# Kernel optimization log

Hardware: AMD Instinct MI355X
Metric: run time of the kernel (lower is better)

## Reference

```python
import jax, jax.numpy as jnp
import numpy as np

N = 131072        # total packed tokens
D = 256           # input_dim
E = 512           # embed_dim
B = 16            # number of batches (len(cu_seqlens)-1)
NLAYERS = 64      # max distinct layer ids per batch


def setup_inputs() -> dict:
    key = jax.random.key(0)
    ks = jax.random.split(key, 8)
    feats = jax.random.normal(ks[0], (N, D), dtype=jnp.float32)
    cu_seqlens = jnp.arange(0, N + 1, N // B, dtype=jnp.int32)  # [B+1]
    layer_ids = jax.random.randint(ks[1], (N,), 0, NLAYERS, dtype=jnp.int32)
    # Linear params stored as [in, out] (y = x @ W + b), matching torch Linear math.
    Wa = jax.random.normal(ks[2], (D, 1), jnp.float32) * 0.05
    ba = jnp.zeros((1,), jnp.float32)
    W1 = jax.random.normal(ks[3], (3 * D, E), jnp.float32) * 0.02
    b1 = jnp.zeros((E,), jnp.float32)
    W2 = jax.random.normal(ks[4], (E, D), jnp.float32) * 0.02
    b2 = jnp.zeros((D,), jnp.float32)
    Wc = jax.random.normal(ks[5], (2 * D, D), jnp.float32) * 0.02
    bc = jnp.zeros((D,), jnp.float32)
    return dict(feats=feats, cu_seqlens=cu_seqlens, layer_ids=layer_ids,
                Wa=Wa, ba=ba, W1=W1, b1=b1, W2=W2, b2=b2, Wc=Wc, bc=bc)


def _forward(feats, cu_seqlens, layer_ids, Wa, ba, W1, b1, W2, b2, Wc, bc):
    n = feats.shape[0]
    nseg = B * NLAYERS
    # batch id of each token from the cumulative sequence lengths
    batch_ids = jnp.searchsorted(cu_seqlens, jnp.arange(n, dtype=jnp.int32), side='right') - 1
    # global (batch, layer) segment id -> vectorizes the per-batch scatter loop
    seg = batch_ids * NLAYERS + layer_ids

    counts = jax.ops.segment_sum(jnp.ones((n,), feats.dtype), seg, num_segments=nseg)  # [nseg]
    sums = jax.ops.segment_sum(feats, seg, num_segments=nseg)                           # [nseg, D]
    avg_pool = sums / jnp.maximum(counts, 1.0)[:, None]
    max_pool = jax.ops.segment_max(feats, seg, num_segments=nseg)
    max_pool = jnp.where(counts[:, None] > 0, max_pool, 0.0)  # empty segments -> 0 (never gathered)

    # attention softmax over all tokens of each batch (dim=0 within the batch slice)
    logits = (feats @ Wa + ba)[:, 0]                                    # [n]
    m = jax.ops.segment_max(logits, batch_ids, num_segments=B)          # [B]
    e = jnp.exp(logits - m[batch_ids])
    z = jax.ops.segment_sum(e, batch_ids, num_segments=B)               # [B]
    w = e / z[batch_ids]                                                # [n]
    attention_pool = jax.ops.segment_sum(feats * w[:, None], seg, num_segments=nseg)

    pooled = jnp.concatenate([avg_pool, max_pool, attention_pool], axis=1)  # [nseg, 3D]
    h = jax.nn.gelu(pooled @ W1 + b1, approximate=False)
    layer_feats = h @ W2 + b2                                               # [nseg, D]

    gathered = layer_feats[seg]                                             # [n, D]
    out = jnp.concatenate([gathered, feats], axis=1) @ Wc + bc              # [n, D]
    return out


def reference(feats, cu_seqlens, layer_ids, Wa, ba, W1, b1, W2, b2, Wc, bc):
    return _forward(feats, cu_seqlens, layer_ids, Wa, ba, W1, b1, W2, b2, Wc, bc)
```

## Files before the change

### kernel.cpp

```cpp
#include <hip/hip_runtime.h>
#include <hip/hip_bf16.h>
#include <math.h>

#define NTOK 131072
#define DIM  256
#define EDIM 512
#define NB   16
#define NL   64
#define NSEG (NB*NL)
#define K3D  768
#define K2D  512
#define HB   64
#define K4CH 256

typedef __attribute__((ext_vector_type(8))) short short8;
typedef __attribute__((ext_vector_type(4))) float f32x4;

static __device__ __forceinline__ unsigned fcode(float x){
  unsigned b = __float_as_uint(x);
  return (b & 0x80000000u) ? ~b : (b | 0x80000000u);
}
static __device__ __forceinline__ float fdecode(unsigned c){
  unsigned b = (c & 0x80000000u) ? (c ^ 0x80000000u) : ~c;
  return __uint_as_float(b);
}
#define NEG_INF_CODE 0x007FFFFFu

static __device__ __forceinline__ short f2bf(float x){
  union { __hip_bfloat16 h; short s; } u; u.h = __float2bfloat16(x); return u.s;
}
static __device__ __forceinline__ float bf2f(short s){
  union { float f; unsigned u; } u; u.u = ((unsigned)(unsigned short)s) << 16; return u.f;
}

__global__ __launch_bounds__(256) void k0_transpose(const float* __restrict__ W1, const float* __restrict__ W2,
                                                    const float* __restrict__ Wc,
                                                    short* __restrict__ W1t, short* __restrict__ W2t,
                                                    short* __restrict__ Wct, unsigned* __restrict__ bmax,
                                                    int* __restrict__ segcnt){
  if (blockIdx.x == 0){
    if (threadIdx.x < NB) bmax[threadIdx.x] = NEG_INF_CODE;
    for (int i = threadIdx.x; i < NSEG; i += 256) segcnt[i] = 0;
  }
  __shared__ short tile[64][65];
  int b = blockIdx.x;
  const float* src; short* dst; int K, N, kt, nt;
  if (b < 96){ src=W1; dst=W1t; K=768; N=512; kt=b/8;  nt=b%8;  }
  else if (b < 128){ int c=b-96;  src=W2; dst=W2t; K=512; N=256; kt=c/4; nt=c%4; }
  else             { int c=b-128; src=Wc; dst=Wct; K=512; N=256; kt=c/4; nt=c%4; }
  int k0 = kt*64, n0 = nt*64;
  for (int e = threadIdx.x; e < 4096; e += 256){
    int r = e >> 6, c = e & 63;
    tile[c][r] = f2bf(src[(size_t)(k0+r)*N + n0 + c]);
  }
  __syncthreads();
  for (int e = threadIdx.x; e < 4096; e += 256){
    int r = e >> 6, c = e & 63;
    dst[(size_t)(n0+r)*K + k0 + c] = tile[r][c];
  }
}

template<int WRITEB>
__global__ __launch_bounds__(256) void k1_logits(const float* __restrict__ feats, const int* __restrict__ cu,
    const int* __restrict__ layer_ids, const float* __restrict__ Wa, const float* __restrict__ ba,
    float* __restrict__ logits, int* __restrict__ seg, unsigned* __restrict__ bmax,
    short* __restrict__ featsb){
  __shared__ int      lcu[NB];
  __shared__ unsigned lbm[NB];
  int tid = threadIdx.x;
  if (tid < NB){ lcu[tid] = cu[tid+1]; lbm[tid] = NEG_INF_CODE; }
  int s = tid & 15;
  int rowoff = tid >> 4;
  float4 w0 = *(const float4*)(Wa + s*4);
  float4 w1 = *(const float4*)(Wa + 64 + s*4);
  float4 w2 = *(const float4*)(Wa + 128 + s*4);
  float4 w3 = *(const float4*)(Wa + 192 + s*4);
  float bav = ba[0];
  __syncthreads();
#pragma unroll
  for (int it = 0; it < 4; ++it){
    int r = (blockIdx.x + it*2048)*16 + rowoff;
    const float4* fp = (const float4*)(feats + (size_t)r*DIM);
    float4 x0 = fp[s], x1 = fp[16+s], x2 = fp[32+s], x3 = fp[48+s];
    float a = x0.x*w0.x + x0.y*w0.y + x0.z*w0.z + x0.w*w0.w
            + x1.x*w1.x + x1.y*w1.y + x1.z*w1.z + x1.w*w1.w
            + x2.x*w2.x + x2.y*w2.y + x2.z*w2.z + x2.w*w2.w
            + x3.x*w3.x + x3.y*w3.y + x3.z*w3.z + x3.w*w3.w;
    if (WRITEB){
      short4* ob = (short4*)(featsb + (size_t)r*DIM);
      short4 v;
      v.x=f2bf(x0.x); v.y=f2bf(x0.y); v.z=f2bf(x0.z); v.w=f2bf(x0.w); ob[s]    = v;
      v.x=f2bf(x1.x); v.y=f2bf(x1.y); v.z=f2bf(x1.z); v.w=f2bf(x1.w); ob[16+s] = v;
      v.x=f2bf(x2.x); v.y=f2bf(x2.y); v.z=f2bf(x2.z); v.w=f2bf(x2.w); ob[32+s] = v;
      v.x=f2bf(x3.x); v.y=f2bf(x3.y); v.z=f2bf(x3.z); v.w=f2bf(x3.w); ob[48+s] = v;
    }
    a += __shfl_xor(a, 1);
    a += __shfl_xor(a, 2);
    a += __shfl_xor(a, 4);
    a += __shfl_xor(a, 8);
    if (s == 0){
      float lg = a + bav;
      logits[r] = lg;
      int b = 0;
#pragma unroll
      for (int j = 0; j < NB-1; ++j) b += (lcu[j] <= r) ? 1 : 0;
      seg[r] = b*NL + layer_ids[r];
      atomicMax(&lbm[b], fcode(lg));
    }
  }
  __syncthreads();
  if (tid < NB && lbm[tid] != NEG_INF_CODE) atomicMax(&bmax[tid], lbm[tid]);
}

__global__ __launch_bounds__(256) void k23_hist_z(const int* __restrict__ seg, int* __restrict__ segcnt,
    const float* __restrict__ logits, const int* __restrict__ cu,
    const unsigned* __restrict__ bmax, float* __restrict__ bz){
  __shared__ int h[NSEG];
  int bid = blockIdx.x;
  if (bid < HB){
    for (int i = threadIdx.x; i < NSEG; i += 256) h[i] = 0;
    __syncthreads();
    int base = bid * (NTOK/HB);
    for (int i = threadIdx.x; i < NTOK/HB; i += 256) atomicAdd(&h[seg[base+i]], 1);
    __syncthreads();
    for (int i = threadIdx.x; i < NSEG; i += 256){ int c = h[i]; if (c) atomicAdd(&segcnt[i], c); }
  } else {
    float* red = (float*)h;
    int b = bid - HB;
    int s = cu[b], e = cu[b+1];
    float m = fdecode(bmax[b]);
    float acc = 0.f;
    for (int i = s + threadIdx.x; i < e; i += 256)
      acc += expf(logits[i] - m);
    red[threadIdx.x] = acc; __syncthreads();
    for (int off = 128; off; off >>= 1){
      if (threadIdx.x < off) red[threadIdx.x] += red[threadIdx.x + off];
      __syncthreads();
    }
    if (threadIdx.x == 0) bz[b] = red[0];
  }
}

__global__ __launch_bounds__(1024) void k3b_scan(const int* __restrict__ segcnt, int* __restrict__ segstart,
                                                 int* __restrict__ cur){
  __shared__ int sc[NSEG];
  int s = threadIdx.x;
  int tot = segcnt[s];
  sc[s] = tot; __syncthreads();
  for (int off = 1; off < NSEG; off <<= 1){
    int v = (s >= off) ? sc[s-off] : 0;
    __syncthreads();
    sc[s] += v;
    __syncthreads();
  }
  int base = sc[s] - tot;
  segstart[s] = base;
  cur[s] = base;
  if (s == 0) segstart[NSEG] = NTOK;
}

__global__ __launch_bounds__(256) void k3c_scatter(const int* __restrict__ seg, int* __restrict__ cur,
                                                   int* __restrict__ sorted){
  __shared__ int h[NSEG];
  for (int i = threadIdx.x; i < NSEG; i += 256) h[i] = 0;
  __syncthreads();
  int base = blockIdx.x * (NTOK/HB);
  for (int i = threadIdx.x; i < NTOK/HB; i += 256) atomicAdd(&h[seg[base+i]], 1);
  __syncthreads();
  for (int i = threadIdx.x; i < NSEG; i += 256){
    int c = h[i];
    if (c) h[i] = atomicAdd(&cur[i], c);
  }
  __syncthreads();
  for (int i = threadIdx.x; i < NTOK/HB; i += 256){
    int sg = seg[base+i];
    int p = atomicAdd(&h[sg], 1);
    sorted[p] = base+i;
  }
}

template<int USEB>
__global__ __launch_bounds__(256) void k4_pool(const float* __restrict__ feats, const short* __restrict__ featsb,
    const int* __restrict__ sorted, const int* __restrict__ segstart,
    const float* __restrict__ logits, const unsigned* __restrict__ bmax, const float* __restrict__ bz,
    short* __restrict__ pooledb){
  __shared__ float redS[4][DIM];
  __shared__ float redM[4][DIM];
  __shared__ float redA[4][DIM];
  __shared__ int   ltok[K4CH];
  __shared__ float lwgt[K4CH];
  int sgi = blockIdx.x;
  int b = sgi >> 6;
  int s = segstart[sgi], e = segstart[sgi+1];
  int cnt = e - s;
  float m = fdecode(bmax[b]);
  float invz = 1.0f / bz[b];
  int lane = threadIdx.x & 63, grp = threadIdx.x >> 6;
  float4 sum = make_float4(0.f,0.f,0.f,0.f), att = make_float4(0.f,0.f,0.f,0.f);
  float4 mx  = make_float4(-INFINITY,-INFINITY,-INFINITY,-INFINITY);
  for (int c0 = s; c0 < e; c0 += K4CH){
    int csz = min(K4CH, e - c0);
    for (int j = threadIdx.x; j < csz; j += 256){
      int t = sorted[c0 + j];
      ltok[j] = t;
      lwgt[j] = expf(logits[t] - m) * invz;
    }
    __syncthreads();
    for (int j = grp; j < csz; j += 4){
      int tok = ltok[j];
      float w = lwgt[j];
      float4 x;
      if (USEB){
        short4 h = *(const short4*)(featsb + (size_t)tok*DIM + lane*4);
        x = make_float4(bf2f(h.x), bf2f(h.y), bf2f(h.z), bf2f(h.w));
      } else {
        x = *(const float4*)(feats + (size_t)tok*DIM + lane*4);
      }
      sum.x += x.x; sum.y += x.y; sum.z += x.z; sum.w += x.w;
      mx.x = fmaxf(mx.x, x.x); mx.y = fmaxf(mx.y, x.y);
      mx.z = fmaxf(mx.z, x.z); mx.w = fmaxf(mx.w, x.w);
      att.x += x.x*w; att.y += x.y*w; att.z += x.z*w; att.w += x.w*w;
    }
    __syncthreads();
  }
  *(float4*)&redS[grp][lane*4] = sum;
  *(float4*)&redM[grp][lane*4] = mx;
  *(float4*)&redA[grp][lane*4] = att;
  __syncthreads();
  int d = threadIdx.x;
  float rs = redS[0][d] + redS[1][d] + redS[2][d] + redS[3][d];
  float rm = fmaxf(fmaxf(redM[0][d], redM[1][d]), fmaxf(redM[2][d], redM[3][d]));
  float ra = redA[0][d] + redA[1][d] + redA[2][d] + redA[3][d];
  float inv = 1.0f / (float)(cnt > 1 ? cnt : 1);
  size_t rb_ = (size_t)sgi * K3D;
  pooledb[rb_ + d]         = f2bf(rs * inv);
  pooledb[rb_ + DIM + d]   = f2bf(cnt > 0 ? rm : 0.f);
  pooledb[rb_ + 2*DIM + d] = f2bf(ra);
}

template<int GELU>
__global__ __launch_bounds__(256) void gemm64(const short* __restrict__ A, const short* __restrict__ Bt,
    const float* __restrict__ bias, short* __restrict__ Cout, int K, int ldc){
  __shared__ short lA[64][40];
  __shared__ short lB[64][40];
  int tid = threadIdx.x;
  int wave = tid >> 6, lane = tid & 63;
  int wm = wave >> 1, wn = wave & 1;
  int rb = blockIdx.x * 64, cb = blockIdx.y * 64;
  int l15 = lane & 15, lg = lane >> 4;
  f32x4 acc[2][2] = {};
  int srow = tid >> 2, skg = tid & 3;
  for (int ks = 0; ks < K; ks += 32){
    __syncthreads();
    *(short8*)&lA[srow][skg*8] = *(const short8*)(A  + (size_t)(rb+srow)*K + ks + skg*8);
    *(short8*)&lB[srow][skg*8] = *(const short8*)(Bt + (size_t)(cb+srow)*K + ks + skg*8);
    __syncthreads();
    short8 af[2], bf[2];
#pragma unroll
    for (int f = 0; f < 2; ++f){
      af[f] = *(const short8*)&lA[wm*32 + f*16 + l15][lg*8];
      bf[f] = *(const short8*)&lB[wn*32 + f*16 + l15][lg*8];
    }
#pragma unroll
    for (int fm = 0; fm < 2; ++fm)
#pragma unroll
      for (int fn = 0; fn < 2; ++fn)
        acc[fm][fn] = __builtin_amdgcn_mfma_f32_16x16x32_bf16(af[fm], bf[fn], acc[fm][fn], 0, 0, 0);
  }
#pragma unroll
  for (int fm = 0; fm < 2; ++fm)
#pragma unroll
    for (int fn = 0; fn < 2; ++fn){
      int col = cb + wn*32 + fn*16 + l15;
      float bcv = bias[col];
#pragma unroll
      for (int r = 0; r < 4; ++r){
        int row = rb + wm*32 + fm*16 + lg*4 + r;
        float v = acc[fm][fn][r] + bcv;
        if (GELU) v = 0.5f * v * (1.0f + erff(v * 0.70710678118f));
        Cout[(size_t)row*ldc + col] = f2bf(v);
      }
    }
}

__global__ __launch_bounds__(256) void k_lfp(const short* __restrict__ A, const short* __restrict__ Bt,
    const float* __restrict__ bias, float* __restrict__ Cout){
  __shared__ short lA[64][40];
  __shared__ short lB[64][40];
  int tid = threadIdx.x;
  int wave = tid >> 6, lane = tid & 63;
  int wm = wave >> 1, wn = wave & 1;
  int rb = blockIdx.x * 64, cb = blockIdx.y * 64;
  int l15 = lane & 15, lg = lane >> 4;
  f32x4 acc[2][2] = {};
  int srow = tid >> 2, skg = tid & 3;
  for (int ks = 0; ks < 256; ks += 32){
    __syncthreads();
    *(short8*)&lA[srow][skg*8] = *(const short8*)(A  + (size_t)(rb+srow)*DIM + ks + skg*8);
    *(short8*)&lB[srow][skg*8] = *(const short8*)(Bt + (size_t)(cb+srow)*K2D + ks + skg*8);
    __syncthreads();
    short8 af[2], bf[2];
#pragma unroll
    for (int f = 0; f < 2; ++f){
      af[f] = *(const short8*)&lA[wm*32 + f*16 + l15][lg*8];
      bf[f] = *(const short8*)&lB[wn*32 + f*16 + l15][lg*8];
    }
#pragma unroll
    for (int fm = 0; fm < 2; ++fm)
#pragma unroll
      for (int fn = 0; fn < 2; ++fn)
        acc[fm][fn] = __builtin_amdgcn_mfma_f32_16x16x32_bf16(af[fm], bf[fn], acc[fm][fn], 0, 0, 0);
  }
#pragma unroll
  for (int fm = 0; fm < 2; ++fm)
#pragma unroll
    for (int fn = 0; fn < 2; ++fn){
      int col = cb + wn*32 + fn*16 + l15;
      float bcv = bias[col];
#pragma unroll
      for (int r = 0; r < 4; ++r){
        int row = rb + wm*32 + fm*16 + lg*4 + r;
        Cout[(size_t)row*DIM + col] = acc[fm][fn][r] + bcv;
      }
    }
}

template<int USEB>
__global__ __launch_bounds__(512, 4) void k5_final(const float* __restrict__ feats,
    const short* __restrict__ featsb, const float* __restrict__ lfp,
    const int* __restrict__ seg, const short* __restrict__ Wct,
    float* __restrict__ out){
  __shared__ short lA[2][128][72];
  __shared__ short lB[2][128][72];
  int tid = threadIdx.x;
  int wave = tid >> 6, lane = tid & 63;
  int wm = wave >> 2, wn = wave & 3;
  int bid = (int)blockIdx.x;
  int swz = (bid & 7) * 256 + (bid >> 3);
  int rb = (swz >> 1) * 128;
  int cb = (swz & 1) * 128;
  int l15 = lane & 15, lg = lane >> 4;
  int arow0 = tid >> 3, arow1 = (tid >> 3) + 64, akg = tid & 7;
  const short* fbp0  = featsb + (size_t)(rb + arow0)*DIM + akg*8;
  const short* fbp1  = featsb + (size_t)(rb + arow1)*DIM + akg*8;
  const float* ffp0  = feats  + (size_t)(rb + arow0)*DIM + akg*8;
  const float* ffp1  = feats  + (size_t)(rb + arow1)*DIM + akg*8;
  const short* wp0 = Wct + (size_t)(cb + arow0)*K2D + 256 + akg*8;
  const short* wp1 = Wct + (size_t)(cb + arow1)*K2D + 256 + akg*8;
  short8 ra0, ra1, rb0, rb1; float4 fa00, fa01, fa10, fa11;
  auto LOAD = [&](int t){
    if (USEB){
      ra0 = *(const short8*)(fbp0 + t*64);
      ra1 = *(const short8*)(fbp1 + t*64);
    } else {
      const float* p0 = ffp0 + (size_t)t*64; fa00 = *(const float4*)p0; fa01 = *(const float4*)(p0+4);
      const float* p1 = ffp1 + (size_t)t*64; fa10 = *(const float4*)p1; fa11 = *(const float4*)(p1+4);
    }
    rb0 = *(const short8*)(wp0 + t*64);
    rb1 = *(const short8*)(wp1 + t*64);
  };
  auto WRITE = [&](int t){
    int buf = t & 1;
    if (!USEB){
      short8 v;
      v[0]=f2bf(fa00.x); v[1]=f2bf(fa00.y); v[2]=f2bf(fa00.z); v[3]=f2bf(fa00.w);
      v[4]=f2bf(fa01.x); v[5]=f2bf(fa01.y); v[6]=f2bf(fa01.z); v[7]=f2bf(fa01.w);
      *(short8*)&lA[buf][arow0][akg*8] = v;
      v[0]=f2bf(fa10.x); v[1]=f2bf(fa10.y); v[2]=f2bf(fa10.z); v[3]=f2bf(fa10.w);
      v[4]=f2bf(fa11.x); v[5]=f2bf(fa11.y); v[6]=f2bf(fa11.z); v[7]=f2bf(fa11.w);
      *(short8*)&lA[buf][arow1][akg*8] = v;
    } else {
      *(short8*)&lA[buf][arow0][akg*8] = ra0;
      *(short8*)&lA[buf][arow1][akg*8] = ra1;
    }
    *(short8*)&lB[buf][arow0][akg*8] = rb0;
    *(short8*)&lB[buf][arow1][akg*8] = rb1;
  };
  f32x4 acc[4][2] = {};
  LOAD(0); WRITE(0); LOAD(1);
  __syncthreads();
  for (int ks = 0; ks < 4; ++ks){
    int cur = ks & 1;
    if (ks < 3) WRITE(ks+1);
    if (ks < 2) LOAD(ks+2);
#pragma unroll
    for (int kk = 0; kk < 2; ++kk){
      short8 af[4], bf[2];
#pragma unroll
      for (int f = 0; f < 4; ++f)
        af[f] = *(const short8*)&lA[cur][wm*64 + f*16 + l15][kk*32 + lg*8];
#pragma unroll
      for (int f = 0; f < 2; ++f)
        bf[f] = *(const short8*)&lB[cur][wn*32 + f*16 + l15][kk*32 + lg*8];
#pragma unroll
      for (int fm = 0; fm < 4; ++fm)
#pragma unroll
        for (int fn = 0; fn < 2; ++fn)
          acc[fm][fn] = __builtin_amdgcn_mfma_f32_16x16x32_bf16(af[fm], bf[fn], acc[fm][fn], 0, 0, 0);
    }
    __syncthreads();
  }
#pragma unroll
  for (int fm = 0; fm < 4; ++fm){
    int rbase = rb + wm*64 + fm*16 + lg*4;
    int4 sg4 = *(const int4*)(seg + rbase);
    int sgs[4] = {sg4.x, sg4.y, sg4.z, sg4.w};
#pragma unroll
    for (int fn = 0; fn < 2; ++fn){
      int col = cb + wn*32 + fn*16 + l15;
#pragma unroll
      for (int r = 0; r < 4; ++r){
        out[(size_t)(rbase+r)*DIM + col] = acc[fm][fn][r] + lfp[(size_t)sgs[r]*DIM + col];
      }
    }
  }
}

extern "C" void kernel_launch(void* const* d_in, const int* in_sizes, int n_in,
                              void* d_out, int out_size, void* d_ws, size_t ws_size,
                              hipStream_t stream){
  const float* feats     = (const float*)d_in[0];
  const int*   cu        = (const int*)d_in[1];
  const int*   layer_ids = (const int*)d_in[2];
  const float* Wa        = (const float*)d_in[3];
  const float* ba        = (const float*)d_in[4];
  const float* W1        = (const float*)d_in[5];
  const float* b1        = (const float*)d_in[6];
  const float* W2        = (const float*)d_in[7];
  const float* b2        = (const float*)d_in[8];
  const float* Wc        = (const float*)d_in[9];
  const float* bc        = (const float*)d_in[10];
  float* out = (float*)d_out;

  char* w = (char*)d_ws;
  auto alloc = [&](size_t bytes)->char*{ char* p = w; w += (bytes + 255) & ~255ull; return p; };
  float*    logits  = (float*)   alloc((size_t)NTOK*4);
  int*      seg     = (int*)     alloc((size_t)NTOK*4);
  int*      sorted  = (int*)     alloc((size_t)NTOK*4);
  int*      segcnt  = (int*)     alloc((size_t)NSEG*4);
  int*      segstart= (int*)     alloc((size_t)(NSEG+1)*4);
  int*      cur     = (int*)     alloc((size_t)NSEG*4);
  unsigned* bmax    = (unsigned*)alloc(NB*4);
  float*    bz      = (float*)   alloc(NB*4);
  short*    W1t     = (short*)   alloc((size_t)512*768*2);
  short*    W2t     = (short*)   alloc((size_t)256*512*2);
  short*    Wct     = (short*)   alloc((size_t)256*512*2);
  short*    pooledb = (short*)   alloc((size_t)NSEG*K3D*2);
  short*    hb      = (short*)   alloc((size_t)NSEG*EDIM*2);
  short*    lfb     = (short*)   alloc((size_t)NSEG*DIM*2);
  float*    lfp     = (float*)   alloc((size_t)NSEG*DIM*4);
  short*    featsb  = (short*)   alloc((size_t)NTOK*DIM*2);
  size_t need = (size_t)(w - (char*)d_ws);
  bool useb = (ws_size >= need);

  k0_transpose<<<dim3(160), dim3(256), 0, stream>>>(W1, W2, Wc, W1t, W2t, Wct, bmax, segcnt);
  if (useb)
    k1_logits<1><<<dim3(2048), dim3(256), 0, stream>>>(feats, cu, layer_ids, Wa, ba, logits, seg, bmax, featsb);
  else
    k1_logits<0><<<dim3(2048), dim3(256), 0, stream>>>(feats, cu, layer_ids, Wa, ba, logits, seg, bmax, featsb);
  k23_hist_z<<<dim3(HB + NB), dim3(256), 0, stream>>>(seg, segcnt, logits, cu, bmax, bz);
  k3b_scan<<<dim3(1), dim3(1024), 0, stream>>>(segcnt, segstart, cur);
  k3c_scatter<<<dim3(HB), dim3(256), 0, stream>>>(seg, cur, sorted);
  if (useb)
    k4_pool<1><<<dim3(NSEG), dim3(256), 0, stream>>>(feats, featsb, sorted, segstart, logits, bmax, bz, pooledb);
  else
    k4_pool<0><<<dim3(NSEG), dim3(256), 0, stream>>>(feats, featsb, sorted, segstart, logits, bmax, bz, pooledb);
  gemm64<1><<<dim3(16, 8), dim3(256), 0, stream>>>(pooledb, W1t, b1, hb, 768, 512);
  gemm64<0><<<dim3(16, 4), dim3(256), 0, stream>>>(hb, W2t, b2, lfb, 512, 256);
  k_lfp<<<dim3(16, 4), dim3(256), 0, stream>>>(lfb, Wct, bc, lfp);
  if (useb)
    k5_final<1><<<dim3(2048), dim3(512), 0, stream>>>(feats, featsb, lfp, seg, Wct, out);
  else
    k5_final<0><<<dim3(2048), dim3(512), 0, stream>>>(feats, featsb, lfp, seg, Wct, out);
}
```

Before: 157.1 us.

## Fuse the three small segment MLP GEMMs into one kernel with LDS-resident intermediates

Replaces the two gemm64 launches and the k_lfp launch with a single k_mlp kernel. Each block takes 16 segment rows and runs W1+GELU, W2 and the Wc projection back to back, keeping the hidden activations in shared memory and streaming weights straight from global memory. This removes two launches and the global round trips for the hidden buffers, but it uses only 64 blocks and reloads the weights per block without LDS tiling. The logits kernel also now computes all four row dot-products before doing the shuffle reductions, to expose more memory-level parallelism.

```diff
diff --git a/kernel.cpp b/kernel.cpp
--- a/kernel.cpp
+++ b/kernel.cpp
@@ -77,15 +77,16 @@
   float4 w3 = *(const float4*)(Wa + 192 + s*4);
   float bav = ba[0];
   __syncthreads();
+  float a[4];
 #pragma unroll
   for (int it = 0; it < 4; ++it){
     int r = (blockIdx.x + it*2048)*16 + rowoff;
     const float4* fp = (const float4*)(feats + (size_t)r*DIM);
     float4 x0 = fp[s], x1 = fp[16+s], x2 = fp[32+s], x3 = fp[48+s];
-    float a = x0.x*w0.x + x0.y*w0.y + x0.z*w0.z + x0.w*w0.w
-            + x1.x*w1.x + x1.y*w1.y + x1.z*w1.z + x1.w*w1.w
-            + x2.x*w2.x + x2.y*w2.y + x2.z*w2.z + x2.w*w2.w
-            + x3.x*w3.x + x3.y*w3.y + x3.z*w3.z + x3.w*w3.w;
+    a[it] = x0.x*w0.x + x0.y*w0.y + x0.z*w0.z + x0.w*w0.w
+          + x1.x*w1.x + x1.y*w1.y + x1.z*w1.z + x1.w*w1.w
+          + x2.x*w2.x + x2.y*w2.y + x2.z*w2.z + x2.w*w2.w
+          + x3.x*w3.x + x3.y*w3.y + x3.z*w3.z + x3.w*w3.w;
     if (WRITEB){
       short4* ob = (short4*)(featsb + (size_t)r*DIM);
       short4 v;
@@ -94,12 +95,17 @@
       v.x=f2bf(x2.x); v.y=f2bf(x2.y); v.z=f2bf(x2.z); v.w=f2bf(x2.w); ob[32+s] = v;
       v.x=f2bf(x3.x); v.y=f2bf(x3.y); v.z=f2bf(x3.z); v.w=f2bf(x3.w); ob[48+s] = v;
     }
-    a += __shfl_xor(a, 1);
-    a += __shfl_xor(a, 2);
-    a += __shfl_xor(a, 4);
-    a += __shfl_xor(a, 8);
+  }
+#pragma unroll
+  for (int it = 0; it < 4; ++it){
+    float v = a[it];
+    v += __shfl_xor(v, 1);
+    v += __shfl_xor(v, 2);
+    v += __shfl_xor(v, 4);
+    v += __shfl_xor(v, 8);
     if (s == 0){
-      float lg = a + bav;
+      int r = (blockIdx.x + it*2048)*16 + rowoff;
+      float lg = v + bav;
       logits[r] = lg;
       int b = 0;
 #pragma unroll
@@ -238,91 +244,88 @@
   pooledb[rb_ + 2*DIM + d] = f2bf(ra);
 }
 
-template<int GELU>
-__global__ __launch_bounds__(256) void gemm64(const short* __restrict__ A, const short* __restrict__ Bt,
-    const float* __restrict__ bias, short* __restrict__ Cout, int K, int ldc){
-  __shared__ short lA[64][40];
-  __shared__ short lB[64][40];
+__global__ __launch_bounds__(256) void k_mlp(const short* __restrict__ pooledb,
+    const short* __restrict__ W1t, const float* __restrict__ b1,
+    const short* __restrict__ W2t, const float* __restrict__ b2,
+    const short* __restrict__ Wct, const float* __restrict__ bc,
+    float* __restrict__ lfp){
+  __shared__ short lA[16][776];
+  __shared__ short lh[16][520];
+  __shared__ short lf[16][264];
   int tid = threadIdx.x;
   int wave = tid >> 6, lane = tid & 63;
-  int wm = wave >> 1, wn = wave & 1;
-  int rb = blockIdx.x * 64, cb = blockIdx.y * 64;
   int l15 = lane & 15, lg = lane >> 4;
-  f32x4 acc[2][2] = {};
-  int srow = tid >> 2, skg = tid & 3;
-  for (int ks = 0; ks < K; ks += 32){
-    __syncthreads();
-    *(short8*)&lA[srow][skg*8] = *(const short8*)(A  + (size_t)(rb+srow)*K + ks + skg*8);
-    *(short8*)&lB[srow][skg*8] = *(const short8*)(Bt + (size_t)(cb+srow)*K + ks + skg*8);
-    __syncthreads();
-    short8 af[2], bf[2];
-#pragma unroll
-    for (int f = 0; f < 2; ++f){
-      af[f] = *(const short8*)&lA[wm*32 + f*16 + l15][lg*8];
-      bf[f] = *(const short8*)&lB[wn*32 + f*16 + l15][lg*8];
-    }
-#pragma unroll
-    for (int fm = 0; fm < 2; ++fm)
-#pragma unroll
-      for (int fn = 0; fn < 2; ++fn)
-        acc[fm][fn] = __builtin_amdgcn_mfma_f32_16x16x32_bf16(af[fm], bf[fn], acc[fm][fn], 0, 0, 0);
-  }
-#pragma unroll
-  for (int fm = 0; fm < 2; ++fm)
-#pragma unroll
-    for (int fn = 0; fn < 2; ++fn){
-      int col = cb + wn*32 + fn*16 + l15;
-      float bcv = bias[col];
+  int r0 = blockIdx.x * 16;
+  for (int i = tid; i < 16*96; i += 256){
+    int row = i / 96, c8 = i % 96;
+    *(short8*)&lA[row][c8*8] = *(const short8*)(pooledb + (size_t)(r0+row)*K3D + c8*8);
+  }
+  __syncthreads();
+  {
+    f32x4 acc[8] = {};
+    int wc = wave * 128;
+    for (int ks = 0; ks < K3D; ks += 32){
+      short8 af = *(const short8*)&lA[l15][ks + lg*8];
+#pragma unroll
+      for (int fn = 0; fn < 8; ++fn){
+        short8 bf = *(const short8*)(W1t + (size_t)(wc + fn*16 + l15)*K3D + ks + lg*8);
+        acc[fn] = __builtin_amdgcn_mfma_f32_16x16x32_bf16(af, bf, acc[fn], 0, 0, 0);
+      }
+    }
+#pragma unroll
+    for (int fn = 0; fn < 8; ++fn){
+      int col = wc + fn*16 + l15;
+      float bcv = b1[col];
 #pragma unroll
       for (int r = 0; r < 4; ++r){
-        int row = rb + wm*32 + fm*16 + lg*4 + r;
-        float v = acc[fm][fn][r] + bcv;
-        if (GELU) v = 0.5f * v * (1.0f + erff(v * 0.70710678118f));
-        Cout[(size_t)row*ldc + col] = f2bf(v);
-      }
-    }
-}
-
-__global__ __launch_bounds__(256) void k_lfp(const short* __restrict__ A, const short* __restrict__ Bt,
-    const float* __restrict__ bias, float* __restrict__ Cout){
-  __shared__ short lA[64][40];
-  __shared__ short lB[64][40];
-  int tid = threadIdx.x;
-  int wave = tid >> 6, lane = tid & 63;
-  int wm = wave >> 1, wn = wave & 1;
-  int rb = blockIdx.x * 64, cb = blockIdx.y * 64;
-  int l15 = lane & 15, lg = lane >> 4;
-  f32x4 acc[2][2] = {};
-  int srow = tid >> 2, skg = tid & 3;
-  for (int ks = 0; ks < 256; ks += 32){
-    __syncthreads();
-    *(short8*)&lA[srow][skg*8] = *(const short8*)(A  + (size_t)(rb+srow)*DIM + ks + skg*8);
-    *(short8*)&lB[srow][skg*8] = *(const short8*)(Bt + (size_t)(cb+srow)*K2D + ks + skg*8);
-    __syncthreads();
-    short8 af[2], bf[2];
-#pragma unroll
-    for (int f = 0; f < 2; ++f){
-      af[f] = *(const short8*)&lA[wm*32 + f*16 + l15][lg*8];
-      bf[f] = *(const short8*)&lB[wn*32 + f*16 + l15][lg*8];
-    }
-#pragma unroll
-    for (int fm = 0; fm < 2; ++fm)
-#pragma unroll
-      for (int fn = 0; fn < 2; ++fn)
-        acc[fm][fn] = __builtin_amdgcn_mfma_f32_16x16x32_bf16(af[fm], bf[fn], acc[fm][fn], 0, 0, 0);
-  }
-#pragma unroll
-  for (int fm = 0; fm < 2; ++fm)
-#pragma unroll
-    for (int fn = 0; fn < 2; ++fn){
-      int col = cb + wn*32 + fn*16 + l15;
-      float bcv = bias[col];
-#pragma unroll
-      for (int r = 0; r < 4; ++r){
-        int row = rb + wm*32 + fm*16 + lg*4 + r;
-        Cout[(size_t)row*DIM + col] = acc[fm][fn][r] + bcv;
-      }
-    }
+        float v = acc[fn][r] + bcv;
+        v = 0.5f * v * (1.0f + erff(v * 0.70710678118f));
+        lh[lg*4 + r][col] = f2bf(v);
+      }
+    }
+  }
+  __syncthreads();
+  {
+    f32x4 acc[4] = {};
+    int wc = wave * 64;
+    for (int ks = 0; ks < EDIM; ks += 32){
+      short8 af = *(const short8*)&lh[l15][ks + lg*8];
+#pragma unroll
+      for (int fn = 0; fn < 4; ++fn){
+        short8 bf = *(const short8*)(W2t + (size_t)(wc + fn*16 + l15)*EDIM + ks + lg*8);
+        acc[fn] = __builtin_amdgcn_mfma_f32_16x16x32_bf16(af, bf, acc[fn], 0, 0, 0);
+      }
+    }
+#pragma unroll
+    for (int fn = 0; fn < 4; ++fn){
+      int col = wc + fn*16 + l15;
+      float bcv = b2[col];
+#pragma unroll
+      for (int r = 0; r < 4; ++r)
+        lf[lg*4 + r][col] = f2bf(acc[fn][r] + bcv);
+    }
+  }
+  __syncthreads();
+  {
+    f32x4 acc[4] = {};
+    int wc = wave * 64;
+    for (int ks = 0; ks < 256; ks += 32){
+      short8 af = *(const short8*)&lf[l15][ks + lg*8];
+#pragma unroll
+      for (int fn = 0; fn < 4; ++fn){
+        short8 bf = *(const short8*)(Wct + (size_t)(wc + fn*16 + l15)*K2D + ks + lg*8);
+        acc[fn] = __builtin_amdgcn_mfma_f32_16x16x32_bf16(af, bf, acc[fn], 0, 0, 0);
+      }
+    }
+#pragma unroll
+    for (int fn = 0; fn < 4; ++fn){
+      int col = wc + fn*16 + l15;
+      float bcv = bc[col];
+#pragma unroll
+      for (int r = 0; r < 4; ++r)
+        lfp[(size_t)(r0 + lg*4 + r)*DIM + col] = acc[fn][r] + bcv;
+    }
+  }
 }
 
 template<int USEB>
@@ -446,8 +449,6 @@
   short*    W2t     = (short*)   alloc((size_t)256*512*2);
   short*    Wct     = (short*)   alloc((size_t)256*512*2);
   short*    pooledb = (short*)   alloc((size_t)NSEG*K3D*2);
-  short*    hb      = (short*)   alloc((size_t)NSEG*EDIM*2);
-  short*    lfb     = (short*)   alloc((size_t)NSEG*DIM*2);
   float*    lfp     = (float*)   alloc((size_t)NSEG*DIM*4);
   short*    featsb  = (short*)   alloc((size_t)NTOK*DIM*2);
   size_t need = (size_t)(w - (char*)d_ws);
@@ -465,9 +466,7 @@
     k4_pool<1><<<dim3(NSEG), dim3(256), 0, stream>>>(feats, featsb, sorted, segstart, logits, bmax, bz, pooledb);
   else
     k4_pool<0><<<dim3(NSEG), dim3(256), 0, stream>>>(feats, featsb, sorted, segstart, logits, bmax, bz, pooledb);
-  gemm64<1><<<dim3(16, 8), dim3(256), 0, stream>>>(pooledb, W1t, b1, hb, 768, 512);
-  gemm64<0><<<dim3(16, 4), dim3(256), 0, stream>>>(hb, W2t, b2, lfb, 512, 256);
-  k_lfp<<<dim3(16, 4), dim3(256), 0, stream>>>(lfb, Wct, bc, lfp);
+  k_mlp<<<dim3(64), dim3(256), 0, stream>>>(pooledb, W1t, b1, W2t, b2, Wct, bc, lfp);
   if (useb)
     k5_final<1><<<dim3(2048), dim3(512), 0, stream>>>(feats, featsb, lfp, seg, Wct, out);
   else
```

Result: slower. 176.2 us (+12.2%).
